# Performance work log

Hardware: AMD Instinct MI355X
Metric: run time of the kernel (lower is better)

Reference implementation:

```python
import jax, jax.numpy as jnp
import numpy as np

LEVELS = 16
FEATURES = 2
HASHMAP_SIZE = 524288
BASE_RES = 16
PER_LEVEL_SCALE = 1.5
HIDDEN = 64
N_POINTS = 2097152
IN_DIM = LEVELS * FEATURES + 3  # 35

# per-level integer resolutions, computed exactly like int(base_res * scale**l)
RES = jnp.asarray([int(BASE_RES * PER_LEVEL_SCALE ** l) for l in range(LEVELS)], dtype=jnp.float32)

P1, P2, P3 = np.int32(73856093), np.int32(19349663), np.int32(83492791)


def hash_coords(coords):
    # coords: [..., 3] int32. int32 multiply wraps, matching torch .int() semantics.
    h = (coords[..., 0] * P1) ^ (coords[..., 1] * P2) ^ (coords[..., 2] * P3)
    return jnp.mod(h, HASHMAP_SIZE)  # Python-style mod -> non-negative


def setup_inputs() -> dict:
    key = jax.random.key(0)
    ks = jax.random.split(key, 8)
    x = jax.random.uniform(ks[0], (N_POINTS, 3), dtype=jnp.float32)
    view_dir = jax.random.normal(ks[1], (N_POINTS, 3), dtype=jnp.float32)
    tables = jax.random.normal(ks[2], (LEVELS, HASHMAP_SIZE, FEATURES), dtype=jnp.float32) * 0.01
    W0 = jax.random.normal(ks[3], (IN_DIM, HIDDEN), dtype=jnp.float32) * (1.0 / np.sqrt(IN_DIM))
    b0 = jnp.zeros((HIDDEN,), jnp.float32)
    W1 = jax.random.normal(ks[4], (HIDDEN, HIDDEN), dtype=jnp.float32) * (1.0 / np.sqrt(HIDDEN))
    b1 = jnp.zeros((HIDDEN,), jnp.float32)
    W2 = jax.random.normal(ks[5], (HIDDEN, 4), dtype=jnp.float32) * (1.0 / np.sqrt(HIDDEN))
    b2 = jnp.zeros((4,), jnp.float32)
    return {"x": x, "view_dir": view_dir, "tables": tables,
            "W0": W0, "b0": b0, "W1": W1, "b1": b1, "W2": W2, "b2": b2}


def reference(x, view_dir, tables, W0, b0, W1, b1, W2, b2):
    # Hash-grid encoding, vectorized over levels: pos [L, N, 3]
    pos = x[None, :, :] * RES[:, None, None]
    pos_floor = jnp.floor(pos).astype(jnp.int32)
    idx = hash_coords(pos_floor)                      # [L, N]
    emb = jax.vmap(lambda t, i: t[i])(tables, idx)    # [L, N, F]
    h = jnp.transpose(emb, (1, 0, 2)).reshape(x.shape[0], LEVELS * FEATURES)
    h = jnp.concatenate([h, view_dir], axis=-1)       # [N, 35]
    h = jax.nn.relu(h @ W0 + b0)
    h = jax.nn.relu(h @ W1 + b1)
    out = h @ W2 + b2                                  # [N, 4]
    rgb = jax.nn.sigmoid(out[..., :3])
    sigma = jax.nn.relu(out[..., 3:4])
    return rgb, sigma
```

## Files before the change

kernel.cpp:

```cpp
#include <hip/hip_runtime.h>
#include <math.h>

#define LEVELS 16
#define HASHMAP_SIZE (1 << 19)
#define N_POINTS 2097152

typedef __attribute__((ext_vector_type(8))) short bf16x8;
typedef __attribute__((ext_vector_type(4))) float f32x4;

__device__ __constant__ float c_res[LEVELS] = {
    16.f, 24.f, 36.f, 54.f, 81.f, 121.f, 182.f, 273.f,
    410.f, 615.f, 922.f, 1383.f, 2075.f, 3113.f, 4670.f, 7006.f};

__device__ __forceinline__ unsigned short f2bf(float f) {
    unsigned u = __builtin_bit_cast(unsigned, f);
    u += 0x7FFFu + ((u >> 16) & 1u);
    return (unsigned short)(u >> 16);
}
__device__ __forceinline__ float bf2f(unsigned short s) {
    unsigned u = ((unsigned)s) << 16;
    return __builtin_bit_cast(float, u);
}
__device__ __forceinline__ unsigned cvt_pk_bf16(float a, float b) {
    unsigned r;
    asm("v_cvt_pk_bf16_f32 %0, %1, %2" : "=v"(r) : "v"(a), "v"(b));
    return r;
}

__device__ __forceinline__ unsigned swz(unsigned row, unsigned colbyte) {
    return row * 128u + (colbyte ^ ((row & 7u) << 4));
}

__device__ __forceinline__ unsigned hash3(float px, float py, float pz, float r) {
    const int ix = (int)floorf(px * r);
    const int iy = (int)floorf(py * r);
    const int iz = (int)floorf(pz * r);
    const unsigned h = (unsigned)ix * 73856093u
                     ^ (unsigned)iy * 19349663u
                     ^ (unsigned)iz * 83492791u;
    return h & (unsigned)(HASHMAP_SIZE - 1);
}

__device__ __forceinline__ bf16x8 load_wfrag(const float* __restrict__ W, int ncols,
                                             int n, int k0, int kmax) {
    bf16x8 r;
    #pragma unroll
    for (int j = 0; j < 8; ++j) {
        const int k = k0 + j;
        const float v = (k < kmax) ? W[k * ncols + n] : 0.f;
        r[j] = (short)f2bf(v);
    }
    return r;
}

__global__ __launch_bounds__(256) void conv_tables(const float* __restrict__ tables,
                                                   unsigned* __restrict__ tabp,
                                                   const float* __restrict__ W0,
                                                   const float* __restrict__ W1,
                                                   unsigned short* __restrict__ w0p,
                                                   unsigned short* __restrict__ w1p) {
    const int t = blockIdx.x * 256 + threadIdx.x;
    if (blockIdx.x < 16) {
        const int i = t;
        const int n = i >> 6, k = i & 63;
        w0p[n * 64 + k] = f2bf((k < 35) ? W0[k * 64 + n] : 0.f);
        w1p[n * 64 + k] = f2bf(W1[k * 64 + n]);
    }
    const float4 a = *reinterpret_cast<const float4*>(tables + (size_t)t * 8);
    const float4 b = *reinterpret_cast<const float4*>(tables + (size_t)t * 8 + 4);
    uint4 o;
    o.x = (unsigned)f2bf(a.x) | ((unsigned)f2bf(a.y) << 16);
    o.y = (unsigned)f2bf(a.z) | ((unsigned)f2bf(a.w) << 16);
    o.z = (unsigned)f2bf(b.x) | ((unsigned)f2bf(b.y) << 16);
    o.w = (unsigned)f2bf(b.z) | ((unsigned)f2bf(b.w) << 16);
    *reinterpret_cast<uint4*>(tabp + (size_t)t * 4) = o;
}

__global__ __launch_bounds__(256, 8) void nerf_gather(
    const float* __restrict__ x,
    const unsigned* __restrict__ tabp,
    unsigned* __restrict__ feat,
    int chunkbase, int chunkpts)
{
    const int b = blockIdx.x;
    const int pair = b & 7;
    const int chunkblk = b >> 3;
    const int l0 = pair, l1 = pair + 8;
    const float r0 = c_res[l0], r1 = c_res[l1];
    const int tid = threadIdx.x;
    const int pbase = chunkblk * 2048;

    unsigned idxA[8], idxB[8];
    #pragma unroll
    for (int i = 0; i < 8; ++i) {
        const int pl = pbase + i * 256 + tid;
        const size_t pg = (size_t)chunkbase + pl;
        const float px = x[pg * 3 + 0];
        const float py = x[pg * 3 + 1];
        const float pz = x[pg * 3 + 2];
        idxA[i] = hash3(px, py, pz, r0);
        idxB[i] = hash3(px, py, pz, r1);
    }
    unsigned gA[8], gB[8];
    #pragma unroll
    for (int i = 0; i < 8; ++i) {
        gA[i] = tabp[(size_t)l0 * HASHMAP_SIZE + idxA[i]];
        gB[i] = tabp[(size_t)l1 * HASHMAP_SIZE + idxB[i]];
    }
    #pragma unroll
    for (int i = 0; i < 8; ++i) {
        const int pl = pbase + i * 256 + tid;
        feat[(size_t)l0 * chunkpts + pl] = gA[i];
        feat[(size_t)l1 * chunkpts + pl] = gB[i];
    }
}

__global__ __launch_bounds__(256, 4) void nerf_mlp(
    const unsigned* __restrict__ feat,
    const float* __restrict__ view_dir,
    const unsigned short* __restrict__ w0p,
    const unsigned short* __restrict__ w1p,
    const float* __restrict__ b0, const float* __restrict__ b1,
    const float* __restrict__ W2, const float* __restrict__ b2,
    float* __restrict__ out,
    int chunkbase, int chunkpts)
{
    __shared__ __align__(16) unsigned short acts[256 * 64];
    char* const actsb = (char*)acts;

    const int tid = threadIdx.x;
    const int gl = blockIdx.x * 256 + tid;
    const size_t gid = (size_t)chunkbase + gl;

    unsigned fw[18];
    #pragma unroll
    for (int l = 0; l < LEVELS; ++l)
        fw[l] = feat[(size_t)l * chunkpts + gl];
    fw[16] = (unsigned)f2bf(view_dir[gid * 3 + 0])
           | ((unsigned)f2bf(view_dir[gid * 3 + 1]) << 16);
    fw[17] = (unsigned)f2bf(view_dir[gid * 3 + 2]);

    {
        const unsigned row = (unsigned)tid;
        #pragma unroll
        for (int c = 0; c < 8; ++c) {
            int4 v;
            if (c < 4)       v = make_int4((int)fw[4*c], (int)fw[4*c+1], (int)fw[4*c+2], (int)fw[4*c+3]);
            else if (c == 4) v = make_int4((int)fw[16], (int)fw[17], 0, 0);
            else             v = make_int4(0, 0, 0, 0);
            *(int4*)(actsb + swz(row, (unsigned)(c * 16))) = v;
        }
    }

    const int lane = tid & 63;
    const int lr = lane & 15;
    const int lg = lane >> 4;
    const unsigned Rbase = (unsigned)(tid & ~63);

    #pragma unroll
    for (int layer = 0; layer < 2; ++layer) {
        const unsigned short* const Wp = layer ? w1p : w0p;
        const float* const bg = layer ? b1 : b0;

        bf16x8 bw[8];
        #pragma unroll
        for (int nt = 0; nt < 4; ++nt)
            #pragma unroll
            for (int ks = 0; ks < 2; ++ks)
                bw[nt * 2 + ks] = *(const bf16x8*)(Wp + (nt * 16 + lr) * 64 + (ks * 32 + lg * 8));

        #pragma unroll
        for (int rt = 0; rt < 4; ++rt) {
            bf16x8 aa[2];
            #pragma unroll
            for (int ks = 0; ks < 2; ++ks) {
                const unsigned row = Rbase + (unsigned)(rt * 16 + lr);
                aa[ks] = *(const bf16x8*)(actsb + swz(row, (unsigned)((ks * 4 + lg) * 16)));
            }
            #pragma unroll
            for (int nt = 0; nt < 4; ++nt) {
                const float bv = bg[nt * 16 + lr];
                f32x4 c = {bv, bv, bv, bv};
                c = __builtin_amdgcn_mfma_f32_16x16x32_bf16(aa[0], bw[nt * 2 + 0], c, 0, 0, 0);
                c = __builtin_amdgcn_mfma_f32_16x16x32_bf16(aa[1], bw[nt * 2 + 1], c, 0, 0, 0);
                const unsigned u01 = cvt_pk_bf16(fmaxf(c[0], 0.f), fmaxf(c[1], 0.f));
                const unsigned u23 = cvt_pk_bf16(fmaxf(c[2], 0.f), fmaxf(c[3], 0.f));
                const unsigned col = (unsigned)(nt * 16 + lr);
                const unsigned rbase = Rbase + (unsigned)(rt * 16 + lg * 4);
                *(unsigned short*)(actsb + swz(rbase + 0, col * 2)) = (unsigned short)u01;
                *(unsigned short*)(actsb + swz(rbase + 1, col * 2)) = (unsigned short)(u01 >> 16);
                *(unsigned short*)(actsb + swz(rbase + 2, col * 2)) = (unsigned short)u23;
                *(unsigned short*)(actsb + swz(rbase + 3, col * 2)) = (unsigned short)(u23 >> 16);
            }
        }
    }

    {
        const bool valid = (lr < 4);
        bf16x8 bw2[2];
        #pragma unroll
        for (int ks = 0; ks < 2; ++ks) {
            if (valid) bw2[ks] = load_wfrag(W2, 4, lr, ks * 32 + lg * 8, 64);
            else       bw2[ks] = bf16x8{0,0,0,0,0,0,0,0};
        }
        const float bc = valid ? b2[lr] : 0.f;

        #pragma unroll
        for (int rt = 0; rt < 4; ++rt) {
            bf16x8 aa[2];
            #pragma unroll
            for (int ks = 0; ks < 2; ++ks) {
                const unsigned row = Rbase + (unsigned)(rt * 16 + lr);
                aa[ks] = *(const bf16x8*)(actsb + swz(row, (unsigned)((ks * 4 + lg) * 16)));
            }
            f32x4 c = {bc, bc, bc, bc};
            c = __builtin_amdgcn_mfma_f32_16x16x32_bf16(aa[0], bw2[0], c, 0, 0, 0);
            c = __builtin_amdgcn_mfma_f32_16x16x32_bf16(aa[1], bw2[1], c, 0, 0, 0);
            if (valid) {
                #pragma unroll
                for (int r = 0; r < 4; ++r) {
                    const unsigned row = Rbase + (unsigned)(rt * 16 + lg * 4 + r);
                    *(float*)(actsb + row * 128u + ((row & 7u) << 4) + (unsigned)lr * 4u) = c[r];
                }
            }
        }
        const unsigned row = (unsigned)tid;
        const f32x4 o = *(const f32x4*)(actsb + row * 128u + ((row & 7u) << 4));
        out[gid * 3 + 0] = 1.f / (1.f + __expf(-o[0]));
        out[gid * 3 + 1] = 1.f / (1.f + __expf(-o[1]));
        out[gid * 3 + 2] = 1.f / (1.f + __expf(-o[2]));
        out[(size_t)N_POINTS * 3 + gid] = fmaxf(o[3], 0.f);
    }
}

__global__ __launch_bounds__(256, 4) void nerf_fused(
    const float* __restrict__ x,
    const float* __restrict__ view_dir,
    const float* __restrict__ tables,
    const float* __restrict__ W0, const float* __restrict__ b0,
    const float* __restrict__ W1, const float* __restrict__ b1,
    const float* __restrict__ W2, const float* __restrict__ b2,
    float* __restrict__ out)
{
    __shared__ __align__(16) unsigned short acts[256 * 64];
    char* const actsb = (char*)acts;
    const int tid = threadIdx.x;
    const int gid = blockIdx.x * 256 + tid;
    const float px = x[gid * 3 + 0], py = x[gid * 3 + 1], pz = x[gid * 3 + 2];

    unsigned idx[LEVELS];
    #pragma unroll
    for (int l = 0; l < LEVELS; ++l) idx[l] = hash3(px, py, pz, c_res[l]);
    float2 f[LEVELS];
    #pragma unroll
    for (int l = 0; l < LEVELS; ++l)
        f[l] = *reinterpret_cast<const float2*>(tables + ((size_t)l * HASHMAP_SIZE + idx[l]) * 2);

    unsigned fw[18];
    #pragma unroll
    for (int l = 0; l < LEVELS; ++l)
        fw[l] = (unsigned)f2bf(f[l].x) | ((unsigned)f2bf(f[l].y) << 16);
    fw[16] = (unsigned)f2bf(view_dir[gid * 3 + 0])
           | ((unsigned)f2bf(view_dir[gid * 3 + 1]) << 16);
    fw[17] = (unsigned)f2bf(view_dir[gid * 3 + 2]);
    {
        const unsigned row = (unsigned)tid;
        #pragma unroll
        for (int c = 0; c < 8; ++c) {
            int4 v;
            if (c < 4)       v = make_int4((int)fw[4*c], (int)fw[4*c+1], (int)fw[4*c+2], (int)fw[4*c+3]);
            else if (c == 4) v = make_int4((int)fw[16], (int)fw[17], 0, 0);
            else             v = make_int4(0, 0, 0, 0);
            *(int4*)(actsb + swz(row, (unsigned)(c * 16))) = v;
        }
    }
    const int lane = tid & 63;
    const int lr = lane & 15;
    const int lg = lane >> 4;
    const unsigned Rbase = (unsigned)(tid & ~63);
    #pragma unroll
    for (int layer = 0; layer < 2; ++layer) {
        const float* const Wg = layer ? W1 : W0;
        const float* const bg = layer ? b1 : b0;
        const int kmax = layer ? 64 : 35;
        bf16x8 bw[8];
        #pragma unroll
        for (int nt = 0; nt < 4; ++nt)
            #pragma unroll
            for (int ks = 0; ks < 2; ++ks)
                bw[nt * 2 + ks] = load_wfrag(Wg, 64, nt * 16 + lr, ks * 32 + lg * 8, kmax);
        #pragma unroll
        for (int rt = 0; rt < 4; ++rt) {
            bf16x8 aa[2];
            #pragma unroll
            for (int ks = 0; ks < 2; ++ks) {
                const unsigned row = Rbase + (unsigned)(rt * 16 + lr);
                aa[ks] = *(const bf16x8*)(actsb + swz(row, (unsigned)((ks * 4 + lg) * 16)));
            }
            #pragma unroll
            for (int nt = 0; nt < 4; ++nt) {
                const float bv = bg[nt * 16 + lr];
                f32x4 c = {bv, bv, bv, bv};
                c = __builtin_amdgcn_mfma_f32_16x16x32_bf16(aa[0], bw[nt * 2 + 0], c, 0, 0, 0);
                c = __builtin_amdgcn_mfma_f32_16x16x32_bf16(aa[1], bw[nt * 2 + 1], c, 0, 0, 0);
                #pragma unroll
                for (int r = 0; r < 4; ++r) {
                    const float v = fmaxf(c[r], 0.f);
                    const unsigned row = Rbase + (unsigned)(rt * 16 + lg * 4 + r);
                    const unsigned col = (unsigned)(nt * 16 + lr);
                    *(unsigned short*)(actsb + swz(row, col * 2)) = f2bf(v);
                }
            }
        }
    }
    {
        float o0 = b2[0], o1 = b2[1], o2 = b2[2], o3 = b2[3];
        const unsigned row = (unsigned)tid;
        #pragma unroll
        for (int c = 0; c < 8; ++c) {
            const bf16x8 v = *(const bf16x8*)(actsb + swz(row, (unsigned)(c * 16)));
            #pragma unroll
            for (int j = 0; j < 8; ++j) {
                const float s = bf2f((unsigned short)v[j]);
                const int k = c * 8 + j;
                o0 += s * W2[k * 4 + 0];
                o1 += s * W2[k * 4 + 1];
                o2 += s * W2[k * 4 + 2];
                o3 += s * W2[k * 4 + 3];
            }
        }
        out[(size_t)gid * 3 + 0] = 1.f / (1.f + __expf(-o0));
        out[(size_t)gid * 3 + 1] = 1.f / (1.f + __expf(-o1));
        out[(size_t)gid * 3 + 2] = 1.f / (1.f + __expf(-o2));
        out[(size_t)N_POINTS * 3 + gid] = fmaxf(o3, 0.f);
    }
}

extern "C" void kernel_launch(void* const* d_in, const int* in_sizes, int n_in,
                              void* d_out, int out_size, void* d_ws, size_t ws_size,
                              hipStream_t stream) {
    (void)in_sizes; (void)n_in; (void)out_size;
    const float* x        = (const float*)d_in[0];
    const float* view_dir = (const float*)d_in[1];
    const float* tables   = (const float*)d_in[2];
    const float* W0       = (const float*)d_in[3];
    const float* b0       = (const float*)d_in[4];
    const float* W1       = (const float*)d_in[5];
    const float* b1       = (const float*)d_in[6];
    const float* W2       = (const float*)d_in[7];
    const float* b2       = (const float*)d_in[8];
    float* out = (float*)d_out;

    const size_t TAB_BYTES = (size_t)LEVELS * HASHMAP_SIZE * 4;
    const size_t WP_BYTES  = 16384;

    int nchunks = 0;
    if      (ws_size >= TAB_BYTES + WP_BYTES + (size_t)N_POINTS * 64) nchunks = 1;
    else if (ws_size >= TAB_BYTES + WP_BYTES + (size_t)N_POINTS * 32) nchunks = 2;
    else if (ws_size >= TAB_BYTES + WP_BYTES + (size_t)N_POINTS * 16) nchunks = 4;

    if (nchunks == 0) {
        nerf_fused<<<N_POINTS / 256, 256, 0, stream>>>(x, view_dir, tables,
                                                       W0, b0, W1, b1, W2, b2, out);
        return;
    }

    unsigned* tabp        = (unsigned*)d_ws;
    unsigned short* w0p   = (unsigned short*)((char*)d_ws + TAB_BYTES);
    unsigned short* w1p   = w0p + 4096;
    unsigned* feat        = (unsigned*)((char*)d_ws + TAB_BYTES + WP_BYTES);
    const int chunkpts = N_POINTS / nchunks;

    conv_tables<<<(LEVELS * HASHMAP_SIZE / 4) / 256, 256, 0, stream>>>(tables, tabp,
                                                                      W0, W1, w0p, w1p);

    for (int c = 0; c < nchunks; ++c) {
        const int base = c * chunkpts;
        nerf_gather<<<8 * (chunkpts / 2048), 256, 0, stream>>>(x, tabp, feat, base, chunkpts);
        nerf_mlp<<<chunkpts / 256, 256, 0, stream>>>(feat, view_dir, w0p, w1p,
                                                     b0, b1, W2, b2, out,
                                                     base, chunkpts);
    }
}
```

Before: 326.1 us.

## Rewrite gather as grid-stride loop with vectorized point loads and nontemporal stores

The gather kernel now runs a fixed grid of 2048 blocks in a grid-stride loop. Each thread handles four consecutive points, loading their coordinates with three float4 loads and writing the gathered features with 16-byte nontemporal stores instead of scalar accesses. The MLP kernel's launch bound is raised from 4 to 5 blocks per CU to allow higher occupancy. Fewer gathers are in flight per thread than in the old 8-way unrolled version, which may reduce latency hiding, and the higher occupancy target could force register spills.

```diff
diff --git a/kernel.cpp b/kernel.cpp
--- a/kernel.cpp
+++ b/kernel.cpp
@@ -7,6 +7,7 @@
 
 typedef __attribute__((ext_vector_type(8))) short bf16x8;
 typedef __attribute__((ext_vector_type(4))) float f32x4;
+typedef __attribute__((ext_vector_type(4))) unsigned u32x4;
 
 __device__ __constant__ float c_res[LEVELS] = {
     16.f, 24.f, 36.f, 54.f, 81.f, 121.f, 182.f, 273.f,
@@ -16,10 +17,6 @@
     unsigned u = __builtin_bit_cast(unsigned, f);
     u += 0x7FFFu + ((u >> 16) & 1u);
     return (unsigned short)(u >> 16);
-}
-__device__ __forceinline__ float bf2f(unsigned short s) {
-    unsigned u = ((unsigned)s) << 16;
-    return __builtin_bit_cast(float, u);
 }
 __device__ __forceinline__ unsigned cvt_pk_bf16(float a, float b) {
     unsigned r;
@@ -76,54 +73,44 @@
     *reinterpret_cast<uint4*>(tabp + (size_t)t * 4) = o;
 }
 
-__global__ __launch_bounds__(256, 8) void nerf_gather(
-    const float* __restrict__ x,
-    const unsigned* __restrict__ tabp,
-    unsigned* __restrict__ feat,
-    int chunkbase, int chunkpts)
+__global__ __launch_bounds__(256, 8) void nerf_gather_k(
+    const float* __restrict__ x, const unsigned* __restrict__ tabp,
+    unsigned* __restrict__ feat, int chunkbase, int chunkpts)
 {
-    const int b = blockIdx.x;
-    const int pair = b & 7;
-    const int chunkblk = b >> 3;
+    const int pair = blockIdx.x & 7;
+    const int bip = blockIdx.x >> 3;
+    const int nbp = gridDim.x / 8;
     const int l0 = pair, l1 = pair + 8;
     const float r0 = c_res[l0], r1 = c_res[l1];
     const int tid = threadIdx.x;
-    const int pbase = chunkblk * 2048;
-
-    unsigned idxA[8], idxB[8];
-    #pragma unroll
-    for (int i = 0; i < 8; ++i) {
-        const int pl = pbase + i * 256 + tid;
+    const int groups = chunkpts >> 2;
+    const int gstride = nbp * 256;
+    const unsigned* __restrict__ t0 = tabp + (size_t)l0 * HASHMAP_SIZE;
+    const unsigned* __restrict__ t1 = tabp + (size_t)l1 * HASHMAP_SIZE;
+    for (int g = bip * 256 + tid; g < groups; g += gstride) {
+        const int pl = g * 4;
         const size_t pg = (size_t)chunkbase + pl;
-        const float px = x[pg * 3 + 0];
-        const float py = x[pg * 3 + 1];
-        const float pz = x[pg * 3 + 2];
-        idxA[i] = hash3(px, py, pz, r0);
-        idxB[i] = hash3(px, py, pz, r1);
-    }
-    unsigned gA[8], gB[8];
-    #pragma unroll
-    for (int i = 0; i < 8; ++i) {
-        gA[i] = tabp[(size_t)l0 * HASHMAP_SIZE + idxA[i]];
-        gB[i] = tabp[(size_t)l1 * HASHMAP_SIZE + idxB[i]];
-    }
-    #pragma unroll
-    for (int i = 0; i < 8; ++i) {
-        const int pl = pbase + i * 256 + tid;
-        feat[(size_t)l0 * chunkpts + pl] = gA[i];
-        feat[(size_t)l1 * chunkpts + pl] = gB[i];
-    }
-}
-
-__global__ __launch_bounds__(256, 4) void nerf_mlp(
-    const unsigned* __restrict__ feat,
-    const float* __restrict__ view_dir,
-    const unsigned short* __restrict__ w0p,
-    const unsigned short* __restrict__ w1p,
+        const float4 xa = *(const float4*)(x + pg * 3 + 0);
+        const float4 xb = *(const float4*)(x + pg * 3 + 4);
+        const float4 xc = *(const float4*)(x + pg * 3 + 8);
+        const unsigned iA0 = hash3(xa.x, xa.y, xa.z, r0), iB0 = hash3(xa.x, xa.y, xa.z, r1);
+        const unsigned iA1 = hash3(xa.w, xb.x, xb.y, r0), iB1 = hash3(xa.w, xb.x, xb.y, r1);
+        const unsigned iA2 = hash3(xb.z, xb.w, xc.x, r0), iB2 = hash3(xb.z, xb.w, xc.x, r1);
+        const unsigned iA3 = hash3(xc.y, xc.z, xc.w, r0), iB3 = hash3(xc.y, xc.z, xc.w, r1);
+        u32x4 gA, gB;
+        gA.x = t0[iA0]; gA.y = t0[iA1]; gA.z = t0[iA2]; gA.w = t0[iA3];
+        gB.x = t1[iB0]; gB.y = t1[iB1]; gB.z = t1[iB2]; gB.w = t1[iB3];
+        __builtin_nontemporal_store(gA, (u32x4*)(feat + (size_t)l0 * chunkpts + pl));
+        __builtin_nontemporal_store(gB, (u32x4*)(feat + (size_t)l1 * chunkpts + pl));
+    }
+}
+
+__global__ __launch_bounds__(256, 5) void nerf_mlp_k(
+    const unsigned* __restrict__ feat, const float* __restrict__ view_dir,
+    const unsigned short* __restrict__ w0p, const unsigned short* __restrict__ w1p,
     const float* __restrict__ b0, const float* __restrict__ b1,
     const float* __restrict__ W2, const float* __restrict__ b2,
-    float* __restrict__ out,
-    int chunkbase, int chunkpts)
+    float* __restrict__ out, int chunkbase, int chunkpts)
 {
     __shared__ __align__(16) unsigned short acts[256 * 64];
     char* const actsb = (char*)acts;
@@ -234,8 +221,7 @@
 }
 
 __global__ __launch_bounds__(256, 4) void nerf_fused(
-    const float* __restrict__ x,
-    const float* __restrict__ view_dir,
+    const float* __restrict__ x, const float* __restrict__ view_dir,
     const float* __restrict__ tables,
     const float* __restrict__ W0, const float* __restrict__ b0,
     const float* __restrict__ W1, const float* __restrict__ b1,
@@ -321,7 +307,7 @@
             const bf16x8 v = *(const bf16x8*)(actsb + swz(row, (unsigned)(c * 16)));
             #pragma unroll
             for (int j = 0; j < 8; ++j) {
-                const float s = bf2f((unsigned short)v[j]);
+                const float s = __builtin_bit_cast(float, ((unsigned)(unsigned short)v[j]) << 16);
                 const int k = c * 8 + j;
                 o0 += s * W2[k * 4 + 0];
                 o1 += s * W2[k * 4 + 1];
@@ -371,14 +357,14 @@
     unsigned* feat        = (unsigned*)((char*)d_ws + TAB_BYTES + WP_BYTES);
     const int chunkpts = N_POINTS / nchunks;
 
-    conv_tables<<<(LEVELS * HASHMAP_SIZE / 4) / 256, 256, 0, stream>>>(tables, tabp,
-                                                                      W0, W1, w0p, w1p);
+    conv_tables<<<(LEVELS * HASHMAP_SIZE / 4) / 256, 256, 0, stream>>>(
+        tables, tabp, W0, W1, w0p, w1p);
 
     for (int c = 0; c < nchunks; ++c) {
         const int base = c * chunkpts;
-        nerf_gather<<<8 * (chunkpts / 2048), 256, 0, stream>>>(x, tabp, feat, base, chunkpts);
-        nerf_mlp<<<chunkpts / 256, 256, 0, stream>>>(feat, view_dir, w0p, w1p,
-                                                     b0, b1, W2, b2, out,
-                                                     base, chunkpts);
-    }
-}
+        nerf_gather_k<<<2048, 256, 0, stream>>>(x, tabp, feat, base, chunkpts);
+        nerf_mlp_k<<<chunkpts / 256, 256, 0, stream>>>(feat, view_dir, w0p, w1p,
+                                                       b0, b1, W2, b2, out,
+                                                       base, chunkpts);
+    }
+}
```

Measured after the change: 428.5 us. 31.4% more time.
